# Optimization experiments

Measured on AMD Instinct MI355X. Metric: run time of the kernel, lower is better.

Reference implementation:

```python
import jax, jax.numpy as jnp
import numpy as np

HEADS = 16
D_MODEL = 1024
D_HEAD = D_MODEL // HEADS


def setup_inputs() -> dict:
    key = jax.random.key(0)
    ks = jax.random.split(key, 12)
    B, S = 4, 2048
    scale = D_MODEL ** -0.5
    inp = {
        "q": jax.random.normal(ks[0], (B, S, D_MODEL), jnp.float32),
        "k": jax.random.normal(ks[1], (B, S, D_MODEL), jnp.float32),
        "v": jax.random.normal(ks[2], (B, S, D_MODEL), jnp.float32),
        # causal mask: True = masked position
        "mask": jnp.triu(jnp.ones((S, S), bool), k=1)[None].repeat(B, axis=0),
        "wq": jax.random.normal(ks[3], (D_MODEL, D_MODEL), jnp.float32) * scale,
        "bq": jnp.zeros((D_MODEL,), jnp.float32),
        "wk": jax.random.normal(ks[4], (D_MODEL, D_MODEL), jnp.float32) * scale,
        "bk": jnp.zeros((D_MODEL,), jnp.float32),
        "wv": jax.random.normal(ks[5], (D_MODEL, D_MODEL), jnp.float32) * scale,
        "bv": jnp.zeros((D_MODEL,), jnp.float32),
        "wo": jax.random.normal(ks[6], (D_MODEL, D_MODEL), jnp.float32) * scale,
        "bo": jnp.zeros((D_MODEL,), jnp.float32),
    }
    return inp


def _split_head(x):
    B, S, _ = x.shape
    return x.reshape(B, S, HEADS, D_HEAD).transpose(0, 2, 1, 3)  # [B,H,S,D]


def reference(q, k, v, mask, wq, bq, wk, bk, wv, bv, wo, bo):
    # linear projections (torch Linear: x @ W^T + b)
    qh = _split_head(q @ wq.T + bq) * (D_HEAD ** -0.5)
    kh = _split_head(k @ wk.T + bk)
    vh = _split_head(v @ wv.T + bv)
    # scores [B,H,Sq,Sk]
    scores = jnp.einsum("bhqd,bhkd->bhqk", qh, kh)
    scores = jnp.where(mask[:, None, :, :], -1e20, scores)
    weights = jax.nn.softmax(scores, axis=-1)  # dropout p=0 in eval
    ctx = jnp.einsum("bhqk,bhkd->bhqd", weights, vh)
    B, H, S, D = ctx.shape
    ctx = ctx.transpose(0, 2, 1, 3).reshape(B, S, H * D)
    return ctx @ wo.T + bo
```

## Files before the change

### kernel.cpp

```cpp
#include <hip/hip_runtime.h>
#include <hip/hip_bf16.h>
#include <cstdint>
#include <cstddef>

typedef unsigned short u16;
typedef unsigned int u32;
using short8  = __attribute__((ext_vector_type(8))) short;
using f32x4   = __attribute__((ext_vector_type(4))) float;
using f32x16  = __attribute__((ext_vector_type(16))) float;
using u32x4   = __attribute__((ext_vector_type(4))) u32;

#define SCALE_Q 0.18033688011112043f

#define WAITVM(N) asm volatile("s_waitcnt vmcnt(" #N ")" ::: "memory")

__device__ inline u16 f2bf(float f) {
  return __builtin_bit_cast(u16, __float2bfloat16(f));
}

__device__ inline u32 cvt_pk_bf16(float a, float b) {
  u32 r;
  asm("v_cvt_pk_bf16_f32 %0, %1, %2" : "=v"(r) : "v"(a), "v"(b));
  return r;
}

__device__ inline f32x4 mfma16(short8 a, short8 b, f32x4 c) {
  return __builtin_amdgcn_mfma_f32_16x16x32_bf16(a, b, c, 0, 0, 0);
}
__device__ inline f32x16 mfma32(short8 a, short8 b, f32x16 c) {
  return __builtin_amdgcn_mfma_f32_32x32x16_bf16(a, b, c, 0, 0, 0);
}

__device__ inline void gload16(const void* g, void* l) {
  __builtin_amdgcn_global_load_lds(
      (const __attribute__((address_space(1))) void*)g,
      (__attribute__((address_space(3))) void*)l,
      16, 0, 0);
}

__global__ __launch_bounds__(256)
void prep(const float* __restrict__ q, const float* __restrict__ k,
          const float* __restrict__ v,
          const float* __restrict__ wq, const float* __restrict__ wk,
          const float* __restrict__ wv, const float* __restrict__ wo,
          u16* __restrict__ Wb, u16* __restrict__ Act) {
  const int c = blockIdx.x * 256 + threadIdx.x;
  const float* src;
  u16* dst;
  float sc = 1.f;
  size_t off;
  if (c < 524288) {
    const int m = c >> 17;
    off = (size_t)(c & 131071) * 8;
    src = (m == 0) ? wq : (m == 1) ? wk : (m == 2) ? wv : wo;
    if (m == 0) sc = SCALE_Q;
    dst = Wb + (size_t)m * 1048576;
  } else {
    const int c2 = c - 524288;
    const int m = c2 >> 20;
    off = (size_t)(c2 & 1048575) * 8;
    src = (m == 0) ? q : (m == 1) ? k : v;
    dst = Act + (size_t)m * 8388608;
  }
  f32x4 a = *(const f32x4*)(src + off);
  f32x4 b = *(const f32x4*)(src + off + 4);
  short8 vv;
#pragma unroll
  for (int j = 0; j < 4; ++j) { vv[j] = (short)f2bf(a[j] * sc); vv[4 + j] = (short)f2bf(b[j] * sc); }
  *(short8*)&dst[off] = vv;
}

struct GemmArgs {
  const u16* Act; const u16* ctx; const u16* Wb;
  const float* bq; const float* bk; const float* bv; const float* bo;
  u16* Qs; u16* Ks; u16* Vs; float* out;
};

__global__ __launch_bounds__(256, 4)
void gemm_proj(GemmArgs ga, int modeBase) {
  const int mode = modeBase + blockIdx.z;
  const int bx = blockIdx.x;
  const int bm = ((bx & 7) << 3) | (bx >> 3);
  const int bn = blockIdx.y;
  const int tid = threadIdx.x;
  const int w = tid >> 6, lane = tid & 63;
  const int wr = w >> 1, wc = w & 1;
  const int l15 = lane & 15, g = lane >> 4;

  const u16* Am = (mode == 3) ? ga.ctx : ga.Act + (size_t)mode * 8388608;
  const u16* Wm = ga.Wb + (size_t)mode * 1048576;
  const float* bias = (mode == 0) ? ga.bq : (mode == 1) ? ga.bk : (mode == 2) ? ga.bv : ga.bo;

  __shared__ u16 As[2][128 * 32];
  __shared__ u16 Bs[2][128 * 32];

  f32x4 acc[4][4] = {};
  const int m0 = bm * 128, n0 = bn * 128;

  const int trow = tid >> 2;
  const int scol = (tid & 3) ^ ((tid >> 3) & 3);
  const int dst0 = w * 512;
  const int dst1 = 2048 + w * 512;

  auto stage = [&](int k0, int slot) {
    gload16(Am + (size_t)(m0 + trow) * 1024 + k0 + scol * 8,      &As[slot][dst0]);
    gload16(Am + (size_t)(m0 + 64 + trow) * 1024 + k0 + scol * 8, &As[slot][dst1]);
    gload16(Wm + (size_t)(n0 + trow) * 1024 + k0 + scol * 8,      &Bs[slot][dst0]);
    gload16(Wm + (size_t)(n0 + 64 + trow) * 1024 + k0 + scol * 8, &Bs[slot][dst1]);
  };

  const int rsw = (l15 >> 1) & 3;

  auto compute = [&](int slot) {
    short8 av[4], bv4[4];
#pragma unroll
    for (int mi = 0; mi < 4; ++mi)
      av[mi] = *(const short8*)&As[slot][(wr * 64 + mi * 16 + l15) * 32 + (g ^ rsw) * 8];
#pragma unroll
    for (int ni = 0; ni < 4; ++ni)
      bv4[ni] = *(const short8*)&Bs[slot][(wc * 64 + ni * 16 + l15) * 32 + (g ^ rsw) * 8];
#pragma unroll
    for (int mi = 0; mi < 4; ++mi)
#pragma unroll
      for (int ni = 0; ni < 4; ++ni)
        acc[mi][ni] = mfma16(av[mi], bv4[ni], acc[mi][ni]);
  };

  stage(0, 0);
  stage(32, 1);

#pragma unroll 2
  for (int t = 0; t < 30; ++t) {
    WAITVM(4);
    __builtin_amdgcn_s_barrier();
    __builtin_amdgcn_sched_barrier(0);
    compute(t & 1);
    __builtin_amdgcn_s_barrier();
    __builtin_amdgcn_sched_barrier(0);
    stage((t + 2) * 32, t & 1);
  }
  WAITVM(4);
  __builtin_amdgcn_s_barrier();
  __builtin_amdgcn_sched_barrier(0);
  compute(0);
  WAITVM(0);
  __builtin_amdgcn_s_barrier();
  __builtin_amdgcn_sched_barrier(0);
  compute(1);

  float bvals[4];
#pragma unroll
  for (int ni = 0; ni < 4; ++ni)
    bvals[ni] = bias[n0 + wc * 64 + ni * 16 + l15] * ((mode == 0) ? SCALE_Q : 1.f);

  if (mode == 3) {
#pragma unroll
    for (int mi = 0; mi < 4; ++mi)
#pragma unroll
      for (int ni = 0; ni < 4; ++ni)
#pragma unroll
        for (int r = 0; r < 4; ++r) {
          const int m = m0 + wr * 64 + mi * 16 + g * 4 + r;
          const int n = n0 + wc * 64 + ni * 16 + l15;
          ga.out[(size_t)m * 1024 + n] = acc[mi][ni][r] + bvals[ni];
        }
  } else {
    u16* O = (mode == 0) ? ga.Qs : (mode == 1) ? ga.Ks : ga.Vs;
#pragma unroll
    for (int mi = 0; mi < 4; ++mi)
#pragma unroll
      for (int ni = 0; ni < 4; ++ni)
#pragma unroll
        for (int r = 0; r < 4; ++r) {
          const int m = m0 + wr * 64 + mi * 16 + g * 4 + r;
          const int n = n0 + wc * 64 + ni * 16 + l15;
          const int b = m >> 11, s = m & 2047, hh = n >> 6, d = n & 63;
          const float val = acc[mi][ni][r] + bvals[ni];
          const size_t base = (size_t)(b * 16 + hh) * 131072;
          size_t idx;
          if (mode == 2) {
            const int sp = (s & ~12) | ((s & 4) << 1) | ((s & 8) >> 1);
            const int kt = sp >> 5, w5 = sp & 31;
            const int j = ((d >> 5) << 1) | (w5 >> 4);
            const int hi2 = (w5 >> 3) & 1, e = w5 & 7;
            idx = base + (size_t)kt * 2048 + j * 512 + hi2 * 256 + (d & 31) * 8 + e;
          } else {
            const int s32 = s >> 5, l31 = s & 31;
            const int t2 = d >> 4, hi2 = (d >> 3) & 1, e = d & 7;
            idx = base + (size_t)s32 * 2048 + t2 * 512 + hi2 * 256 + l31 * 8 + e;
          }
          O[idx] = f2bf(val);
        }
  }
}

__global__ __launch_bounds__(256)
void attn_fwd(const u16* __restrict__ Qs, const u16* __restrict__ Ks,
              const u16* __restrict__ Vs, u16* __restrict__ ctx) {
  const int bh = blockIdx.x;
  const int qt = 15 - blockIdx.y;
  const int tid = threadIdx.x;
  const int w = tid >> 6, lane = tid & 63;
  const int l31 = lane & 31, hi = lane >> 5;

  const u16* Qb = Qs + (size_t)bh * 131072;
  const u16* Kb = Ks + (size_t)bh * 131072 + lane * 8;
  const u16* Vb = Vs + (size_t)bh * 131072 + lane * 8;
  const int b = bh >> 4, hh = bh & 15;

  const int qw0 = qt * 128 + w * 32;
  const int nkt = (qw0 >> 5) + 1;
  const int qrow = qw0 + l31;

  short8 qf[4];
  {
    const u16* qp = Qb + (size_t)(qw0 >> 5) * 2048 + lane * 8;
#pragma unroll
    for (int t = 0; t < 4; ++t) qf[t] = *(const short8*)(qp + t * 512);
  }

  f32x16 oacc0 = {}, oacc1 = {};
  float lsum = 0.f;

  auto body = [&](const short8* kf, const short8* vf, int kt, bool last) {
    f32x16 st = {};
    __builtin_amdgcn_s_setprio(1);
    st = mfma32(kf[0], qf[0], st);
    st = mfma32(kf[1], qf[1], st);
    st = mfma32(kf[2], qf[2], st);
    st = mfma32(kf[3], qf[3], st);
    __builtin_amdgcn_s_setprio(0);
    if (last) {
#pragma unroll
      for (int r = 0; r < 16; ++r) {
        const int ka = kt * 32 + (r & 3) + 8 * (r >> 2) + 4 * hi;
        if (ka > qrow) st[r] = -1e30f;
      }
    }
    float p[16];
#pragma unroll
    for (int r = 0; r < 16; ++r) p[r] = __builtin_amdgcn_exp2f(st[r]);
    {
      float s0 = (p[0] + p[1]) + (p[2] + p[3]);
      float s1 = (p[4] + p[5]) + (p[6] + p[7]);
      float s2 = (p[8] + p[9]) + (p[10] + p[11]);
      float s3 = (p[12] + p[13]) + (p[14] + p[15]);
      lsum += (s0 + s1) + (s2 + s3);
    }
    u32x4 a0, a1;
#pragma unroll
    for (int v2 = 0; v2 < 4; ++v2) {
      a0[v2] = cvt_pk_bf16(p[2 * v2], p[2 * v2 + 1]);
      a1[v2] = cvt_pk_bf16(p[8 + 2 * v2], p[9 + 2 * v2]);
    }
    const short8 pb0 = __builtin_bit_cast(short8, a0);
    const short8 pb1 = __builtin_bit_cast(short8, a1);
    __builtin_amdgcn_s_setprio(1);
    oacc0 = mfma32(vf[0], pb0, oacc0);
    oacc0 = mfma32(vf[1], pb1, oacc0);
    oacc1 = mfma32(vf[2], pb0, oacc1);
    oacc1 = mfma32(vf[3], pb1, oacc1);
    __builtin_amdgcn_s_setprio(0);
  };

  short8 kA[4], vA[4], kB[4], vB[4];
#pragma unroll
  for (int t = 0; t < 4; ++t) {
    kA[t] = *(const short8*)(Kb + t * 512);
    vA[t] = *(const short8*)(Vb + t * 512);
  }

  for (int kt = 0; ; ) {
    const bool lastA = (kt + 1 == nkt);
    if (!lastA) {
      const u16* kp = Kb + (size_t)(kt + 1) * 2048;
      const u16* vp = Vb + (size_t)(kt + 1) * 2048;
#pragma unroll
      for (int t = 0; t < 4; ++t) {
        kB[t] = *(const short8*)(kp + t * 512);
        vB[t] = *(const short8*)(vp + t * 512);
      }
    }
    body(kA, vA, kt, lastA);
    if (lastA) break;
    ++kt;
    const bool lastB = (kt + 1 == nkt);
    if (!lastB) {
      const u16* kp = Kb + (size_t)(kt + 1) * 2048;
      const u16* vp = Vb + (size_t)(kt + 1) * 2048;
#pragma unroll
      for (int t = 0; t < 4; ++t) {
        kA[t] = *(const short8*)(kp + t * 512);
        vA[t] = *(const short8*)(vp + t * 512);
      }
    }
    body(kB, vB, kt, lastB);
    if (lastB) break;
    ++kt;
  }

  lsum += __shfl_xor(lsum, 32);
  const float inv = __builtin_amdgcn_rcpf(lsum);

  u16* crow = ctx + ((size_t)(b * 2048 + qrow)) * 1024 + hh * 64;
#pragma unroll
  for (int r = 0; r < 16; r += 2) {
    const int d0 = (r & 3) + 8 * (r >> 2) + 4 * hi;
    *(u32*)&crow[d0]      = cvt_pk_bf16(oacc0[r] * inv, oacc0[r + 1] * inv);
    *(u32*)&crow[32 + d0] = cvt_pk_bf16(oacc1[r] * inv, oacc1[r + 1] * inv);
  }
}

extern "C" void kernel_launch(void* const* d_in, const int* in_sizes, int n_in,
                              void* d_out, int out_size, void* d_ws, size_t ws_size,
                              hipStream_t stream) {
  const float* q  = (const float*)d_in[0];
  const float* k  = (const float*)d_in[1];
  const float* v  = (const float*)d_in[2];
  const float* wq = (const float*)d_in[4];
  const float* bq = (const float*)d_in[5];
  const float* wk = (const float*)d_in[6];
  const float* bk = (const float*)d_in[7];
  const float* wv = (const float*)d_in[8];
  const float* bv = (const float*)d_in[9];
  const float* wo = (const float*)d_in[10];
  const float* bo = (const float*)d_in[11];

  char* ws = (char*)d_ws;
  const size_t WBSZ  = (size_t)4 * 1048576 * sizeof(u16);
  const size_t ACTSZ = (size_t)3 * 8388608 * sizeof(u16);
  const size_t SZ    = (size_t)64 * 131072 * sizeof(u16);
  u16* Wb  = (u16*)(ws);
  u16* Act = (u16*)(ws + WBSZ);
  u16* Qs  = (u16*)(ws + WBSZ + ACTSZ);
  u16* Ks  = (u16*)(ws + WBSZ + ACTSZ + SZ);
  u16* Vs  = (u16*)(ws + WBSZ + ACTSZ + 2 * SZ);
  u16* ctx = (u16*)(ws + WBSZ + ACTSZ + 3 * SZ);

  GemmArgs ga;
  ga.Act = Act; ga.ctx = ctx; ga.Wb = Wb;
  ga.bq = bq; ga.bk = bk; ga.bv = bv; ga.bo = bo;
  ga.Qs = Qs; ga.Ks = Ks; ga.Vs = Vs; ga.out = (float*)d_out;

  prep<<<dim3(14336), dim3(256), 0, stream>>>(q, k, v, wq, wk, wv, wo, Wb, Act);
  gemm_proj<<<dim3(64, 8, 3), dim3(256), 0, stream>>>(ga, 0);
  attn_fwd<<<dim3(64, 16), dim3(256), 0, stream>>>(Qs, Ks, Vs, ctx);
  gemm_proj<<<dim3(64, 8, 1), dim3(256), 0, stream>>>(ga, 3);
}
```

Baseline: 190.7 us.

## Double GEMM K-tile depth to 64 with new XOR swizzle and fewer barriers

The projection GEMM now stages 64-wide K tiles instead of 32, halving the number of loop iterations and barrier pairs. The shared-memory layout is reorganised with an 8-way XOR swizzle over row&7, and each stage issues eight global-to-LDS loads. LDS use doubles to 64 KB per block, and launch bounds drop occupancy to 3 blocks per CU, trading occupancy for less synchronisation overhead per unit of work.

New measurement: 176.2 us. -7.6%, faster.

```diff
diff --git a/kernel.cpp b/kernel.cpp
--- a/kernel.cpp
+++ b/kernel.cpp
@@ -76,7 +76,7 @@
   u16* Qs; u16* Ks; u16* Vs; float* out;
 };
 
-__global__ __launch_bounds__(256, 4)
+__global__ __launch_bounds__(256, 3)
 void gemm_proj(GemmArgs ga, int modeBase) {
   const int mode = modeBase + blockIdx.z;
   const int bx = blockIdx.x;
@@ -91,55 +91,61 @@
   const u16* Wm = ga.Wb + (size_t)mode * 1048576;
   const float* bias = (mode == 0) ? ga.bq : (mode == 1) ? ga.bk : (mode == 2) ? ga.bv : ga.bo;
 
-  __shared__ u16 As[2][128 * 32];
-  __shared__ u16 Bs[2][128 * 32];
+  __shared__ u16 As[2][128 * 64];
+  __shared__ u16 Bs[2][128 * 64];
 
   f32x4 acc[4][4] = {};
   const int m0 = bm * 128, n0 = bn * 128;
 
-  const int trow = tid >> 2;
-  const int scol = (tid & 3) ^ ((tid >> 3) & 3);
-  const int dst0 = w * 512;
-  const int dst1 = 2048 + w * 512;
+  const int r_lo = lane >> 3;
+  const int sc8 = ((lane & 7) ^ (lane >> 3)) * 8;
 
   auto stage = [&](int k0, int slot) {
-    gload16(Am + (size_t)(m0 + trow) * 1024 + k0 + scol * 8,      &As[slot][dst0]);
-    gload16(Am + (size_t)(m0 + 64 + trow) * 1024 + k0 + scol * 8, &As[slot][dst1]);
-    gload16(Wm + (size_t)(n0 + trow) * 1024 + k0 + scol * 8,      &Bs[slot][dst0]);
-    gload16(Wm + (size_t)(n0 + 64 + trow) * 1024 + k0 + scol * 8, &Bs[slot][dst1]);
+#pragma unroll
+    for (int i = 0; i < 4; ++i) {
+      const int row = i * 32 + w * 8 + r_lo;
+      const int db = i * 2048 + w * 512;
+      gload16(Am + (size_t)(m0 + row) * 1024 + k0 + sc8, &As[slot][db]);
+      gload16(Wm + (size_t)(n0 + row) * 1024 + k0 + sc8, &Bs[slot][db]);
+    }
   };
 
-  const int rsw = (l15 >> 1) & 3;
-
   auto compute = [&](int slot) {
-    short8 av[4], bv4[4];
-#pragma unroll
-    for (int mi = 0; mi < 4; ++mi)
-      av[mi] = *(const short8*)&As[slot][(wr * 64 + mi * 16 + l15) * 32 + (g ^ rsw) * 8];
-#pragma unroll
-    for (int ni = 0; ni < 4; ++ni)
-      bv4[ni] = *(const short8*)&Bs[slot][(wc * 64 + ni * 16 + l15) * 32 + (g ^ rsw) * 8];
-#pragma unroll
-    for (int mi = 0; mi < 4; ++mi)
-#pragma unroll
-      for (int ni = 0; ni < 4; ++ni)
-        acc[mi][ni] = mfma16(av[mi], bv4[ni], acc[mi][ni]);
+#pragma unroll
+    for (int kk = 0; kk < 2; ++kk) {
+      short8 av[4], bv4[4];
+#pragma unroll
+      for (int mi = 0; mi < 4; ++mi) {
+        const int row = wr * 64 + mi * 16 + l15;
+        av[mi] = *(const short8*)&As[slot][row * 64 + ((((kk << 2) | g)) ^ (row & 7)) * 8];
+      }
+#pragma unroll
+      for (int ni = 0; ni < 4; ++ni) {
+        const int row = wc * 64 + ni * 16 + l15;
+        bv4[ni] = *(const short8*)&Bs[slot][row * 64 + ((((kk << 2) | g)) ^ (row & 7)) * 8];
+      }
+#pragma unroll
+      for (int mi = 0; mi < 4; ++mi)
+#pragma unroll
+        for (int ni = 0; ni < 4; ++ni)
+          acc[mi][ni] = mfma16(av[mi], bv4[ni], acc[mi][ni]);
+    }
   };
 
   stage(0, 0);
-  stage(32, 1);
+  stage(64, 1);
 
 #pragma unroll 2
-  for (int t = 0; t < 30; ++t) {
-    WAITVM(4);
+  for (int t = 0; t < 14; ++t) {
+    WAITVM(8);
     __builtin_amdgcn_s_barrier();
     __builtin_amdgcn_sched_barrier(0);
     compute(t & 1);
     __builtin_amdgcn_s_barrier();
     __builtin_amdgcn_sched_barrier(0);
-    stage((t + 2) * 32, t & 1);
-  }
-  WAITVM(4);
+    stage((t + 2) * 64, t & 1);
+  }
+  WAITVM(8);
   __builtin_amdgcn_s_barrier();
   __builtin_amdgcn_sched_barrier(0);
   compute(0);
```
